# Kernel optimization log

Hardware: AMD Instinct MI355X
Metric: run time of the kernel (lower is better)

## Reference

```python
import jax, jax.numpy as jnp
import numpy as np

N = 50000       # nodes
E = 800000      # edges
F_IN = 128      # num_features
DIM = 64        # dim
D0 = 4 * DIM    # layer-0 width = 256
G = 256         # num graphs
EPS_BN = 1e-5


def _init_linear(key, fan_in, fan_out, bias=True):
    k1, k2 = jax.random.split(key)
    W = jax.random.normal(k1, (fan_in, fan_out), jnp.float32) * (1.0 / np.sqrt(fan_in))
    if bias:
        b = jax.random.normal(k2, (fan_out,), jnp.float32) * 0.01
        return W, b
    return W


def setup_inputs() -> dict:
    key = jax.random.key(0)
    ks = jax.random.split(key, 16)
    x = jax.random.normal(ks[0], (N, F_IN), jnp.float32)
    edge_index = jax.random.randint(ks[1], (2, E), 0, N, jnp.int32)
    edge_attr = jax.random.normal(ks[2], (E, 1), jnp.float32)
    batch = jnp.sort(jax.random.randint(ks[3], (N,), 0, G, jnp.int32))
    # conv0: in F_IN -> out D0, heads=1, edge_dim=1
    Wq0, bq0 = _init_linear(ks[4], F_IN, D0)
    Wk0, bk0 = _init_linear(ks[5], F_IN, D0)
    Wv0, bv0 = _init_linear(ks[6], F_IN, D0)
    We0 = _init_linear(ks[7], 1, D0, bias=False)   # lin_edge has no bias in PyG
    Ws0, bs0 = _init_linear(ks[8], F_IN, D0)       # lin_skip (root weight)
    # conv1: in D0 -> out DIM
    Wq1, bq1 = _init_linear(ks[9], D0, DIM)
    Wk1, bk1 = _init_linear(ks[10], D0, DIM)
    Wv1, bv1 = _init_linear(ks[11], D0, DIM)
    We1 = _init_linear(ks[12], 1, DIM, bias=False)
    Ws1, bs1 = _init_linear(ks[13], D0, DIM)
    # BatchNorm affine params
    gamma0 = jnp.ones((D0,), jnp.float32)
    beta0 = jnp.zeros((D0,), jnp.float32)
    gamma1 = jnp.ones((DIM,), jnp.float32)
    beta1 = jnp.zeros((DIM,), jnp.float32)
    return dict(x=x, edge_index=edge_index, edge_attr=edge_attr, batch=batch,
                Wq0=Wq0, bq0=bq0, Wk0=Wk0, bk0=bk0, Wv0=Wv0, bv0=bv0, We0=We0, Ws0=Ws0, bs0=bs0,
                gamma0=gamma0, beta0=beta0,
                Wq1=Wq1, bq1=bq1, Wk1=Wk1, bk1=bk1, Wv1=Wv1, bv1=bv1, We1=We1, Ws1=Ws1, bs1=bs1,
                gamma1=gamma1, beta1=beta1)


def _transformer_conv(x, edge_index, edge_attr, Wq, bq, Wk, bk, Wv, bv, We, Ws, bs):
    # PyG TransformerConv, heads=1, concat=True, root_weight=True, beta=False
    src, dst = edge_index[0], edge_index[1]
    n, d = x.shape[0], Wq.shape[1]
    q = x @ Wq + bq            # [N, d]
    k = x @ Wk + bk
    v = x @ Wv + bv
    e = edge_attr @ We          # [E, d]
    ke = k[src] + e             # key_j + edge embedding
    logits = jnp.sum(q[dst] * ke, axis=-1) / jnp.sqrt(jnp.asarray(d, jnp.float32))  # [E]
    # scatter-softmax over incoming edges of each dst node
    m = jax.ops.segment_max(logits, dst, num_segments=n)
    p = jnp.exp(logits - m[dst])
    s = jax.ops.segment_sum(p, dst, num_segments=n)
    alpha = p / (s[dst] + 1e-16)
    msg = (v[src] + e) * alpha[:, None]              # [E, d]
    out = jax.ops.segment_sum(msg, dst, num_segments=n)
    return out + x @ Ws + bs                          # root/skip connection


def _batch_norm(x, gamma, beta):
    mu = jnp.mean(x, axis=0)
    var = jnp.mean(jnp.square(x - mu), axis=0)  # biased var (torch training mode)
    return gamma * (x - mu) * jax.lax.rsqrt(var + EPS_BN) + beta


def _global_mean_pool(x, batch, num_graphs):
    s = jax.ops.segment_sum(x, batch, num_segments=num_graphs)
    c = jax.ops.segment_sum(jnp.ones((x.shape[0],), x.dtype), batch, num_segments=num_graphs)
    return s / jnp.maximum(c, 1.0)[:, None]


def reference(x, edge_index, edge_attr, batch,
              Wq0, bq0, Wk0, bk0, Wv0, bv0, We0, Ws0, bs0, gamma0, beta0,
              Wq1, bq1, Wk1, bk1, Wv1, bv1, We1, Ws1, bs1, gamma1, beta1):
    h0 = _batch_norm(_transformer_conv(x, edge_index, edge_attr,
                                       Wq0, bq0, Wk0, bk0, Wv0, bv0, We0, Ws0, bs0),
                     gamma0, beta0)                  # [N, D0]
    h1 = _batch_norm(_transformer_conv(h0, edge_index, edge_attr,
                                       Wq1, bq1, Wk1, bk1, Wv1, bv1, We1, Ws1, bs1),
                     gamma1, beta1)                  # [N, DIM]
    xpool = jnp.concatenate([_global_mean_pool(h0, batch, G),
                             _global_mean_pool(h1, batch, G)], axis=1)  # [G, D0+DIM]
    xs = jnp.concatenate([h0, h1], axis=1)                               # [N, D0+DIM]
    return (xpool, xs)
```

## Files before the change

### kernel.cpp

```cpp
#include <hip/hip_runtime.h>

constexpr int NN = 50000;
constexpr int NE = 800000;
constexpr int F_IN = 128;
constexpr int D0 = 256;
constexpr int D1 = 64;
constexpr int NG = 256;
constexpr float EPS_BN = 1e-5f;

typedef __attribute__((ext_vector_type(8))) short bf16x8;
typedef __attribute__((ext_vector_type(4))) float f32x4;
typedef __attribute__((ext_vector_type(8))) ushort u16x8;
typedef __attribute__((ext_vector_type(4))) ushort u16x4;

__device__ inline ushort f2bf(float f) {
    uint32_t u = __float_as_uint(f);
    uint32_t r = u + 0x7fff + ((u >> 16) & 1);
    return (ushort)(r >> 16);
}
__device__ inline float bf2f(ushort b) {
    return __uint_as_float((uint32_t)b << 16);
}

__global__ __launch_bounds__(256) void k_hist(const int* __restrict__ ei, int* __restrict__ cnt) {
    int e = blockIdx.x * 256 + threadIdx.x;
    if (e < NE) atomicAdd(&cnt[ei[NE + e]], 1);
}

__global__ __launch_bounds__(256) void k_scan1(const int* __restrict__ cnt,
                                               int* __restrict__ offs,
                                               int* __restrict__ bsum) {
    __shared__ int lds[256];
    int idx = blockIdx.x * 256 + threadIdx.x;
    int v = (idx < NN) ? cnt[idx] : 0;
    lds[threadIdx.x] = v;
    __syncthreads();
    #pragma unroll
    for (int off = 1; off < 256; off <<= 1) {
        int add = (threadIdx.x >= off) ? lds[threadIdx.x - off] : 0;
        __syncthreads();
        lds[threadIdx.x] += add;
        __syncthreads();
    }
    if (idx < NN) offs[idx] = lds[threadIdx.x] - v;
    if (threadIdx.x == 255) bsum[blockIdx.x] = lds[255];
}

__global__ __launch_bounds__(256) void k_scan2(const int* __restrict__ bsum,
                                               int* __restrict__ boff, int nblk) {
    __shared__ int lds[256];
    int v = (threadIdx.x < nblk) ? bsum[threadIdx.x] : 0;
    lds[threadIdx.x] = v;
    __syncthreads();
    #pragma unroll
    for (int off = 1; off < 256; off <<= 1) {
        int add = (threadIdx.x >= off) ? lds[threadIdx.x - off] : 0;
        __syncthreads();
        lds[threadIdx.x] += add;
        __syncthreads();
    }
    if (threadIdx.x < nblk) boff[threadIdx.x] = lds[threadIdx.x] - v;
}

__global__ __launch_bounds__(256) void k_scan3(int* __restrict__ offs,
                                               const int* __restrict__ boff,
                                               int* __restrict__ cursor) {
    int idx = blockIdx.x * 256 + threadIdx.x;
    if (idx < NN) {
        int o = offs[idx] + boff[blockIdx.x];
        offs[idx] = o;
        cursor[idx] = o;
    }
    if (idx == 0) offs[NN] = NE;
}

__global__ __launch_bounds__(256) void k_scatter(const int* __restrict__ ei,
                                                 const float* __restrict__ ea,
                                                 int* __restrict__ cursor,
                                                 int2* __restrict__ sedge) {
    int e = blockIdx.x * 256 + threadIdx.x;
    if (e < NE) {
        int d = ei[NE + e];
        int pos = atomicAdd(&cursor[d], 1);
        sedge[pos] = make_int2(ei[e], __float_as_int(ea[e]));
    }
}

__global__ __launch_bounds__(256) void k_f2bf4(const float* __restrict__ in,
                                               ushort* __restrict__ out, int n4) {
    for (int i = blockIdx.x * 256 + threadIdx.x; i < n4; i += gridDim.x * 256) {
        float4 v = *reinterpret_cast<const float4*>(&in[(size_t)i * 4]);
        ushort4 o;
        o.x = f2bf(v.x); o.y = f2bf(v.y); o.z = f2bf(v.z); o.w = f2bf(v.w);
        *reinterpret_cast<ushort4*>(&out[(size_t)i * 4]) = o;
    }
}

struct WPrep {
    const float* src[8];
    ushort* dst[8];
    int K[8];
    int D[8];
};
__global__ __launch_bounds__(256) void k_wprep(WPrep p) {
    int m = blockIdx.y;
    int K = p.K[m], D = p.D[m];
    int n = K * D;
    for (int idx = blockIdx.x * 256 + threadIdx.x; idx < n; idx += gridDim.x * 256) {
        int c = idx / K, k = idx - c * K;
        p.dst[m][idx] = f2bf(p.src[m][(size_t)k * D + c]);
    }
}

template<int K, int DOUT>
__global__ __launch_bounds__(256) void k_gemm_mfma(
    const ushort* __restrict__ Xb, const ushort* __restrict__ Wt,
    const float* __restrict__ B0, const float* __restrict__ B1,
    const float* __restrict__ B2, const float* __restrict__ B3,
    float* __restrict__ Oq, ushort* __restrict__ Okv,
    float* __restrict__ Oh)
{
    constexpr int BM = 128, BN = 64, BK = 32;
    __shared__ ushort Xs[BM][BK + 8];
    __shared__ ushort Wss[BN][BK + 8];

    int row0 = blockIdx.x * BM;
    int col0 = blockIdx.y * BN;
    int mat = col0 / DOUT;
    int mcol0 = col0 - mat * DOUT;
    const float* Bb = (mat == 0) ? B0 : (mat == 1) ? B1 : (mat == 2) ? B2 : B3;

    int t = threadIdx.x;
    int wid = t >> 6, lane = t & 63;
    int wr = wid >> 1, wc = wid & 1;
    int lr = lane & 15, lk = lane >> 4;

    f32x4 acc[4][2] = {};

    for (int k0 = 0; k0 < K; k0 += BK) {
        #pragma unroll
        for (int i = 0; i < 2; ++i) {
            int slot = t + i * 256;
            int r = slot >> 2, c8 = slot & 3;
            int gr = row0 + r;
            uint4 val = make_uint4(0, 0, 0, 0);
            if (gr < NN) val = *reinterpret_cast<const uint4*>(&Xb[(size_t)gr * K + k0 + c8 * 8]);
            *reinterpret_cast<uint4*>(&Xs[r][c8 * 8]) = val;
        }
        {
            int r = t >> 2, c8 = t & 3;
            uint4 val = *reinterpret_cast<const uint4*>(&Wt[(size_t)(col0 + r) * K + k0 + c8 * 8]);
            *reinterpret_cast<uint4*>(&Wss[r][c8 * 8]) = val;
        }
        __syncthreads();
        bf16x8 a[4], b[2];
        #pragma unroll
        for (int m = 0; m < 4; ++m)
            a[m] = *reinterpret_cast<const bf16x8*>(&Xs[wr * 64 + m * 16 + lr][lk * 8]);
        #pragma unroll
        for (int n = 0; n < 2; ++n)
            b[n] = *reinterpret_cast<const bf16x8*>(&Wss[wc * 32 + n * 16 + lr][lk * 8]);
        #pragma unroll
        for (int m = 0; m < 4; ++m)
            #pragma unroll
            for (int n = 0; n < 2; ++n)
                acc[m][n] = __builtin_amdgcn_mfma_f32_16x16x32_bf16(a[m], b[n], acc[m][n], 0, 0, 0);
        __syncthreads();
    }

    #pragma unroll
    for (int m = 0; m < 4; ++m) {
        #pragma unroll
        for (int n = 0; n < 2; ++n) {
            int gcol = mcol0 + wc * 32 + n * 16 + lr;
            float bias = Bb[gcol];
            #pragma unroll
            for (int r = 0; r < 4; ++r) {
                int grow = row0 + wr * 64 + m * 16 + lk * 4 + r;
                if (grow >= NN) continue;
                float vv = acc[m][n][r] + bias;
                if (mat == 0) Oq[(size_t)grow * DOUT + gcol] = vv;
                else if (mat == 1) Okv[(size_t)grow * (2 * DOUT) + gcol] = f2bf(vv);
                else if (mat == 2) Okv[(size_t)grow * (2 * DOUT) + DOUT + gcol] = f2bf(vv);
                else Oh[(size_t)grow * DOUT + gcol] = vv;
            }
        }
    }
}

template<int D>
__global__ __launch_bounds__(256) void k_attn(
    const float* __restrict__ q, const ushort* __restrict__ kvb,
    const float* __restrict__ We,
    const int2* __restrict__ sedge,
    const int* __restrict__ offs,
    float* __restrict__ hout)
{
    int wave = threadIdx.x >> 6;
    int lane = threadIdx.x & 63;
    int node = blockIdx.x * 4 + wave;
    if (node >= NN) return;
    int start = offs[node], stop = offs[node + 1];

    if constexpr (D == 256) {
        constexpr float scale = 0.0625f;
        int g = lane >> 5, sl = lane & 31;
        float q8[8], wel8[8];
        {
            float4 qa = *reinterpret_cast<const float4*>(&q[(size_t)node * 256 + sl * 8]);
            float4 qb = *reinterpret_cast<const float4*>(&q[(size_t)node * 256 + sl * 8 + 4]);
            q8[0] = qa.x; q8[1] = qa.y; q8[2] = qa.z; q8[3] = qa.w;
            q8[4] = qb.x; q8[5] = qb.y; q8[6] = qb.z; q8[7] = qb.w;
            float4 wa = *reinterpret_cast<const float4*>(&We[sl * 8]);
            float4 wb = *reinterpret_cast<const float4*>(&We[sl * 8 + 4]);
            wel8[0] = wa.x; wel8[1] = wa.y; wel8[2] = wa.z; wel8[3] = wa.w;
            wel8[4] = wb.x; wel8[5] = wb.y; wel8[6] = wb.z; wel8[7] = wb.w;
        }
        float qWe = 0.f;
        #pragma unroll
        for (int c = 0; c < 8; ++c) qWe = fmaf(q8[c], wel8[c], qWe);
        #pragma unroll
        for (int o = 1; o <= 16; o <<= 1) qWe += __shfl_xor(qWe, o);

        int niter = (stop - start + 1) >> 1;
        float acc8[8] = {};
        float ssum = 0.f, sse = 0.f;

        bool val0, val1; int2 se0, se1;
        u16x8 ku0, vu0, ku1, vu1;
        auto LOAD = [&](int j, bool& val, int2& se, u16x8& ku, u16x8& vu) {
            int idx = start + 2 * j + g;
            val = idx < stop;
            int e = val ? idx : 0;
            se = sedge[e];
            const ushort* base = &kvb[(size_t)se.x * 512 + sl * 8];
            ku = *reinterpret_cast<const u16x8*>(base);
            vu = *reinterpret_cast<const u16x8*>(base + 256);
        };
        LOAD(0, val0, se0, ku0, vu0);
        LOAD(1, val1, se1, ku1, vu1);

        for (int j = 0; j < niter; ++j) {
            bool val2; int2 se2; u16x8 ku2, vu2;
            LOAD(j + 2, val2, se2, ku2, vu2);
            float dot = 0.f;
            #pragma unroll
            for (int c = 0; c < 8; ++c) dot = fmaf(q8[c], bf2f((ushort)ku0[c]), dot);
            #pragma unroll
            for (int o = 1; o <= 16; o <<= 1) dot += __shfl_xor(dot, o);
            float eav = __int_as_float(se0.y);
            float p = val0 ? __expf((dot + eav * qWe) * scale) : 0.f;
            ssum += p;
            sse = fmaf(p, eav, sse);
            #pragma unroll
            for (int c = 0; c < 8; ++c) acc8[c] = fmaf(p, bf2f((ushort)vu0[c]), acc8[c]);
            val0 = val1; se0 = se1; ku0 = ku1; vu0 = vu1;
            val1 = val2; se1 = se2; ku1 = ku2; vu1 = vu2;
        }
        #pragma unroll
        for (int c = 0; c < 8; ++c) acc8[c] = fmaf(sse, wel8[c], acc8[c]);
        ssum += __shfl_xor(ssum, 32);
        #pragma unroll
        for (int c = 0; c < 8; ++c) acc8[c] += __shfl_xor(acc8[c], 32);
        float inv = 1.0f / (ssum + 1e-16f);
        float o4[4];
        #pragma unroll
        for (int c = 0; c < 4; ++c) o4[c] = g ? acc8[4 + c] : acc8[c];
        float* hp = &hout[(size_t)node * 256 + sl * 8 + g * 4];
        float4 cur = *reinterpret_cast<float4*>(hp);
        cur.x += o4[0] * inv; cur.y += o4[1] * inv;
        cur.z += o4[2] * inv; cur.w += o4[3] * inv;
        *reinterpret_cast<float4*>(hp) = cur;
    } else {
        constexpr float scale = 0.125f;
        int g = lane >> 4, sl = lane & 15;
        float q4[4], wel4[4];
        {
            float4 qa = *reinterpret_cast<const float4*>(&q[(size_t)node * 64 + sl * 4]);
            q4[0] = qa.x; q4[1] = qa.y; q4[2] = qa.z; q4[3] = qa.w;
            float4 wa = *reinterpret_cast<const float4*>(&We[sl * 4]);
            wel4[0] = wa.x; wel4[1] = wa.y; wel4[2] = wa.z; wel4[3] = wa.w;
        }
        float qWe = 0.f;
        #pragma unroll
        for (int c = 0; c < 4; ++c) qWe = fmaf(q4[c], wel4[c], qWe);
        #pragma unroll
        for (int o = 1; o <= 8; o <<= 1) qWe += __shfl_xor(qWe, o);

        int niter = (stop - start + 3) >> 2;
        float acc4[4] = {};
        float ssum = 0.f, sse = 0.f;

        bool val0, val1; int2 se0, se1;
        u16x4 ku0, vu0, ku1, vu1;
        auto LOAD = [&](int j, bool& val, int2& se, u16x4& ku, u16x4& vu) {
            int idx = start + 4 * j + g;
            val = idx < stop;
            int e = val ? idx : 0;
            se = sedge[e];
            const ushort* base = &kvb[(size_t)se.x * 128 + sl * 4];
            ku = *reinterpret_cast<const u16x4*>(base);
            vu = *reinterpret_cast<const u16x4*>(base + 64);
        };
        LOAD(0, val0, se0, ku0, vu0);
        LOAD(1, val1, se1, ku1, vu1);

        for (int j = 0; j < niter; ++j) {
            bool val2; int2 se2; u16x4 ku2, vu2;
            LOAD(j + 2, val2, se2, ku2, vu2);
            float dot = 0.f;
            #pragma unroll
            for (int c = 0; c < 4; ++c) dot = fmaf(q4[c], bf2f((ushort)ku0[c]), dot);
            #pragma unroll
            for (int o = 1; o <= 8; o <<= 1) dot += __shfl_xor(dot, o);
            float eav = __int_as_float(se0.y);
            float p = val0 ? __expf((dot + eav * qWe) * scale) : 0.f;
            ssum += p;
            sse = fmaf(p, eav, sse);
            #pragma unroll
            for (int c = 0; c < 4; ++c) acc4[c] = fmaf(p, bf2f((ushort)vu0[c]), acc4[c]);
            val0 = val1; se0 = se1; ku0 = ku1; vu0 = vu1;
            val1 = val2; se1 = se2; ku1 = ku2; vu1 = vu2;
        }
        #pragma unroll
        for (int c = 0; c < 4; ++c) acc4[c] = fmaf(sse, wel4[c], acc4[c]);
        ssum += __shfl_xor(ssum, 16);
        ssum += __shfl_xor(ssum, 32);
        #pragma unroll
        for (int c = 0; c < 4; ++c) {
            acc4[c] += __shfl_xor(acc4[c], 16);
            acc4[c] += __shfl_xor(acc4[c], 32);
        }
        float inv = 1.0f / (ssum + 1e-16f);
        float av = acc4[0];
        av = (g == 1) ? acc4[1] : av;
        av = (g == 2) ? acc4[2] : av;
        av = (g == 3) ? acc4[3] : av;
        hout[(size_t)node * 64 + sl * 4 + g] += av * inv;
    }
}

template<int D>
__global__ __launch_bounds__(256) void k_bnstats(const float* __restrict__ h,
                                                 float* __restrict__ sums,
                                                 int rows_per_block) {
    constexpr int NSUB = 256 / D;
    int col = threadIdx.x % D;
    int sub = threadIdx.x / D;
    int r0 = blockIdx.x * rows_per_block;
    int r1 = min(r0 + rows_per_block, NN);
    float s = 0.f, ss = 0.f;
    for (int r = r0 + sub; r < r1; r += NSUB) {
        float x = h[(size_t)r * D + col];
        s += x; ss += x * x;
    }
    atomicAdd(&sums[col], s);
    atomicAdd(&sums[D + col], ss);
}

template<int D>
__global__ void k_bnfin(const float* __restrict__ sums,
                        const float* __restrict__ gamma, const float* __restrict__ beta,
                        float* __restrict__ ab) {
    int c = threadIdx.x;
    if (c >= D) return;
    float mean = sums[c] / (float)NN;
    float var = sums[D + c] / (float)NN - mean * mean;
    float a = gamma[c] * rsqrtf(var + EPS_BN);
    ab[c] = a;
    ab[D + c] = beta[c] - mean * a;
}

__global__ __launch_bounds__(256) void k_bnapply0(float* __restrict__ h,
                                                  const float* __restrict__ ab,
                                                  float* __restrict__ xs,
                                                  ushort* __restrict__ h0b) {
    int idx = blockIdx.x * 256 + threadIdx.x;
    int n = idx >> 6, c4 = idx & 63;
    float4 x4 = *reinterpret_cast<float4*>(&h[(size_t)idx * 4]);
    float4 a4 = *reinterpret_cast<const float4*>(&ab[c4 * 4]);
    float4 b4 = *reinterpret_cast<const float4*>(&ab[256 + c4 * 4]);
    float4 r;
    r.x = a4.x * x4.x + b4.x; r.y = a4.y * x4.y + b4.y;
    r.z = a4.z * x4.z + b4.z; r.w = a4.w * x4.w + b4.w;
    *reinterpret_cast<float4*>(&xs[(size_t)n * 320 + c4 * 4]) = r;
    ushort4 o;
    o.x = f2bf(r.x); o.y = f2bf(r.y); o.z = f2bf(r.z); o.w = f2bf(r.w);
    *reinterpret_cast<ushort4*>(&h0b[(size_t)idx * 4]) = o;
}

__global__ __launch_bounds__(256) void k_bnapply1(const float* __restrict__ h,
                                                  const float* __restrict__ ab,
                                                  float* __restrict__ xs) {
    int idx = blockIdx.x * 256 + threadIdx.x;
    int n = idx >> 4, c4 = idx & 15;
    float4 x4 = *reinterpret_cast<const float4*>(&h[(size_t)idx * 4]);
    float4 a4 = *reinterpret_cast<const float4*>(&ab[c4 * 4]);
    float4 b4 = *reinterpret_cast<const float4*>(&ab[64 + c4 * 4]);
    float4 r;
    r.x = a4.x * x4.x + b4.x; r.y = a4.y * x4.y + b4.y;
    r.z = a4.z * x4.z + b4.z; r.w = a4.w * x4.w + b4.w;
    *reinterpret_cast<float4*>(&xs[(size_t)n * 320 + 256 + c4 * 4]) = r;
}

__global__ __launch_bounds__(256) void k_pool(const float* __restrict__ xs,
                                              const int* __restrict__ batch,
                                              float* __restrict__ xpool) {
    int g = blockIdx.x;
    __shared__ int se[2];
    if (threadIdx.x < 2) {
        int target = g + threadIdx.x;
        int lo = 0, hi = NN;
        while (lo < hi) {
            int mid = (lo + hi) >> 1;
            if (batch[mid] < target) lo = mid + 1; else hi = mid;
        }
        se[threadIdx.x] = lo;
    }
    __syncthreads();
    int start = se[0], stop = se[1];
    float cnt = fmaxf((float)(stop - start), 1.0f);
    for (int c = threadIdx.x; c < 320; c += 256) {
        float s = 0.f;
        for (int r = start; r < stop; ++r) s += xs[(size_t)r * 320 + c];
        xpool[(size_t)g * 320 + c] = s / cnt;
    }
}

extern "C" void kernel_launch(void* const* d_in, const int* in_sizes, int n_in,
                              void* d_out, int out_size, void* d_ws, size_t ws_size,
                              hipStream_t stream) {
    const float* x     = (const float*)d_in[0];
    const int*   ei    = (const int*)d_in[1];
    const float* ea    = (const float*)d_in[2];
    const int*   batch = (const int*)d_in[3];
    const float *Wq0 = (const float*)d_in[4],  *bq0 = (const float*)d_in[5];
    const float *Wk0 = (const float*)d_in[6],  *bk0 = (const float*)d_in[7];
    const float *Wv0 = (const float*)d_in[8],  *bv0 = (const float*)d_in[9];
    const float *We0 = (const float*)d_in[10];
    const float *Ws0 = (const float*)d_in[11], *bs0 = (const float*)d_in[12];
    const float *gamma0 = (const float*)d_in[13], *beta0 = (const float*)d_in[14];
    const float *Wq1 = (const float*)d_in[15], *bq1 = (const float*)d_in[16];
    const float *Wk1 = (const float*)d_in[17], *bk1 = (const float*)d_in[18];
    const float *Wv1 = (const float*)d_in[19], *bv1 = (const float*)d_in[20];
    const float *We1 = (const float*)d_in[21];
    const float *Ws1 = (const float*)d_in[22], *bs1 = (const float*)d_in[23];
    const float *gamma1 = (const float*)d_in[24], *beta1 = (const float*)d_in[25];

    char* ws = (char*)d_ws;
    size_t off = 0;
    auto alloc = [&](size_t bytes) -> char* {
        char* p = ws + off;
        off += (bytes + 255) & ~(size_t)255;
        return p;
    };
    float*  q0   = (float*)alloc((size_t)NN * D0 * 4);
    ushort* kv0  = (ushort*)alloc((size_t)NN * 2 * D0 * 2);
    float*  h0   = (float*)alloc((size_t)NN * D0 * 4);
    ushort* xbuf = (ushort*)alloc((size_t)NN * D0 * 2);
    int2*  sedge = (int2*)alloc((size_t)NE * 8);
    int*   cnt    = (int*)alloc((size_t)(NN + 1) * 4);
    int*   offs   = (int*)alloc((size_t)(NN + 1) * 4);
    int*   cursor = (int*)alloc((size_t)(NN + 1) * 4);
    int*   bsum   = (int*)alloc(256 * 4);
    int*   boff   = (int*)alloc(256 * 4);
    float* sums0  = (float*)alloc(2 * D0 * 4);
    float* ab0    = (float*)alloc(2 * D0 * 4);
    float* sums1  = (float*)alloc(2 * D1 * 4);
    float* ab1    = (float*)alloc(2 * D1 * 4);
    ushort* wt0   = (ushort*)alloc((size_t)4 * D0 * F_IN * 2);
    ushort* wt1   = (ushort*)alloc((size_t)4 * D1 * D0 * 2);

    ushort* xb  = xbuf;
    ushort* h0b = xbuf;

    float*  q1  = q0;
    ushort* kv1 = kv0;
    float*  h1  = h0;

    float* xpool = (float*)d_out;
    float* xs = (float*)d_out + (size_t)NG * 320;

    const int NBLK = (NN + 255) / 256;
    const int BN_BLK = (NN + 63) / 64;

    hipMemsetAsync(cnt, 0, (NN + 1) * 4, stream);
    k_hist<<<(NE + 255) / 256, 256, 0, stream>>>(ei, cnt);
    k_scan1<<<NBLK, 256, 0, stream>>>(cnt, offs, bsum);
    k_scan2<<<1, 256, 0, stream>>>(bsum, boff, NBLK);
    k_scan3<<<NBLK, 256, 0, stream>>>(offs, boff, cursor);
    k_scatter<<<(NE + 255) / 256, 256, 0, stream>>>(ei, ea, cursor, sedge);

    k_f2bf4<<<2048, 256, 0, stream>>>(x, xb, NN * F_IN / 4);
    WPrep wp;
    wp.src[0] = Wq0; wp.src[1] = Wk0; wp.src[2] = Wv0; wp.src[3] = Ws0;
    wp.src[4] = Wq1; wp.src[5] = Wk1; wp.src[6] = Wv1; wp.src[7] = Ws1;
    for (int m = 0; m < 4; ++m) { wp.K[m] = F_IN; wp.D[m] = D0; wp.dst[m] = wt0 + (size_t)m * D0 * F_IN; }
    for (int m = 0; m < 4; ++m) { wp.K[4+m] = D0; wp.D[4+m] = D1; wp.dst[4+m] = wt1 + (size_t)m * D1 * D0; }
    k_wprep<<<dim3(64, 8), 256, 0, stream>>>(wp);

    k_gemm_mfma<F_IN, D0><<<dim3((NN + 127) / 128, 16), 256, 0, stream>>>(
        xb, wt0, bq0, bk0, bv0, bs0, q0, kv0, h0);
    k_attn<D0><<<(NN + 3) / 4, 256, 0, stream>>>(q0, kv0, We0, sedge, offs, h0);
    hipMemsetAsync(sums0, 0, 2 * D0 * 4, stream);
    k_bnstats<D0><<<BN_BLK, 256, 0, stream>>>(h0, sums0, 64);
    k_bnfin<D0><<<1, D0, 0, stream>>>(sums0, gamma0, beta0, ab0);
    k_bnapply0<<<(NN * 64 + 255) / 256, 256, 0, stream>>>(h0, ab0, xs, h0b);

    k_gemm_mfma<D0, D1><<<dim3((NN + 127) / 128, 4), 256, 0, stream>>>(
        h0b, wt1, bq1, bk1, bv1, bs1, q1, kv1, h1);
    k_attn<D1><<<(NN + 3) / 4, 256, 0, stream>>>(q1, kv1, We1, sedge, offs, h1);
    hipMemsetAsync(sums1, 0, 2 * D1 * 4, stream);
    k_bnstats<D1><<<BN_BLK, 256, 0, stream>>>(h1, sums1, 64);
    k_bnfin<D1><<<1, D1, 0, stream>>>(sums1, gamma1, beta1, ab1);
    k_bnapply1<<<(NN * 16 + 255) / 256, 256, 0, stream>>>(h1, ab1, xs);

    k_pool<<<NG, 256, 0, stream>>>(xs, batch, xpool);
}
```

Baseline: 768.6 us.

## Store Q in bf16, interleave layer-1 K/V, widen GEMM tile, tile weight transpose

The query projection output is now written and read as bf16 instead of fp32, which halves Q traffic between the GEMM and attention kernels. In layer 1, K and V are interleaved per 4-column group so each lane gathers both with a single 16-byte load per edge instead of two 8-byte loads. The layer-0 GEMM uses a 128-wide N tile to improve reuse of the X tile, and the weight transpose/convert now goes through an LDS tile so global accesses are coalesced. Rounding Q to bf16 adds some numerical error in the attention logits.

```diff
diff --git a/kernel.cpp b/kernel.cpp
--- a/kernel.cpp
+++ b/kernel.cpp
@@ -105,22 +105,38 @@
 __global__ __launch_bounds__(256) void k_wprep(WPrep p) {
     int m = blockIdx.y;
     int K = p.K[m], D = p.D[m];
-    int n = K * D;
-    for (int idx = blockIdx.x * 256 + threadIdx.x; idx < n; idx += gridDim.x * 256) {
-        int c = idx / K, k = idx - c * K;
-        p.dst[m][idx] = f2bf(p.src[m][(size_t)k * D + c]);
-    }
-}
-
-template<int K, int DOUT>
+    int ntx = K >> 5, nty = D >> 5;
+    int tile = blockIdx.x;
+    if (tile >= ntx * nty) return;
+    int tk = (tile % ntx) << 5;
+    int tc = (tile / ntx) << 5;
+    __shared__ ushort lds[32][33];
+    int tx = threadIdx.x & 31, ty = threadIdx.x >> 5;
+    const float* src = p.src[m];
+    ushort* dst = p.dst[m];
+    #pragma unroll
+    for (int i = 0; i < 4; ++i) {
+        int k = tk + ty + i * 8;
+        lds[ty + i * 8][tx] = f2bf(src[(size_t)k * D + tc + tx]);
+    }
+    __syncthreads();
+    #pragma unroll
+    for (int i = 0; i < 4; ++i) {
+        int c = tc + ty + i * 8;
+        dst[(size_t)c * K + tk + tx] = lds[tx][ty + i * 8];
+    }
+}
+
+template<int K, int DOUT, int BN>
 __global__ __launch_bounds__(256) void k_gemm_mfma(
     const ushort* __restrict__ Xb, const ushort* __restrict__ Wt,
     const float* __restrict__ B0, const float* __restrict__ B1,
     const float* __restrict__ B2, const float* __restrict__ B3,
-    float* __restrict__ Oq, ushort* __restrict__ Okv,
+    ushort* __restrict__ Oqb, ushort* __restrict__ Okv,
     float* __restrict__ Oh)
 {
-    constexpr int BM = 128, BN = 64, BK = 32;
+    constexpr int BM = 128, BK = 32;
+    constexpr int NB = BN / 32;
     __shared__ ushort Xs[BM][BK + 8];
     __shared__ ushort Wss[BN][BK + 8];
 
@@ -135,7 +151,7 @@
     int wr = wid >> 1, wc = wid & 1;
     int lr = lane & 15, lk = lane >> 4;
 
-    f32x4 acc[4][2] = {};
+    f32x4 acc[4][NB] = {};
 
     for (int k0 = 0; k0 < K; k0 += BK) {
         #pragma unroll
@@ -147,23 +163,25 @@
             if (gr < NN) val = *reinterpret_cast<const uint4*>(&Xb[(size_t)gr * K + k0 + c8 * 8]);
             *reinterpret_cast<uint4*>(&Xs[r][c8 * 8]) = val;
         }
-        {
-            int r = t >> 2, c8 = t & 3;
+        #pragma unroll
+        for (int i = 0; i < (BN * 4) / 256; ++i) {
+            int slot = t + i * 256;
+            int r = slot >> 2, c8 = slot & 3;
             uint4 val = *reinterpret_cast<const uint4*>(&Wt[(size_t)(col0 + r) * K + k0 + c8 * 8]);
             *reinterpret_cast<uint4*>(&Wss[r][c8 * 8]) = val;
         }
         __syncthreads();
-        bf16x8 a[4], b[2];
+        bf16x8 a[4], b[NB];
         #pragma unroll
         for (int m = 0; m < 4; ++m)
             a[m] = *reinterpret_cast<const bf16x8*>(&Xs[wr * 64 + m * 16 + lr][lk * 8]);
         #pragma unroll
-        for (int n = 0; n < 2; ++n)
-            b[n] = *reinterpret_cast<const bf16x8*>(&Wss[wc * 32 + n * 16 + lr][lk * 8]);
+        for (int n = 0; n < NB; ++n)
+            b[n] = *reinterpret_cast<const bf16x8*>(&Wss[wc * (BN / 2) + n * 16 + lr][lk * 8]);
         #pragma unroll
         for (int m = 0; m < 4; ++m)
             #pragma unroll
-            for (int n = 0; n < 2; ++n)
+            for (int n = 0; n < NB; ++n)
                 acc[m][n] = __builtin_amdgcn_mfma_f32_16x16x32_bf16(a[m], b[n], acc[m][n], 0, 0, 0);
         __syncthreads();
     }
@@ -171,18 +189,23 @@
     #pragma unroll
     for (int m = 0; m < 4; ++m) {
         #pragma unroll
-        for (int n = 0; n < 2; ++n) {
-            int gcol = mcol0 + wc * 32 + n * 16 + lr;
+        for (int n = 0; n < NB; ++n) {
+            int gcol = mcol0 + wc * (BN / 2) + n * 16 + lr;
             float bias = Bb[gcol];
             #pragma unroll
             for (int r = 0; r < 4; ++r) {
                 int grow = row0 + wr * 64 + m * 16 + lk * 4 + r;
                 if (grow >= NN) continue;
                 float vv = acc[m][n][r] + bias;
-                if (mat == 0) Oq[(size_t)grow * DOUT + gcol] = vv;
-                else if (mat == 1) Okv[(size_t)grow * (2 * DOUT) + gcol] = f2bf(vv);
-                else if (mat == 2) Okv[(size_t)grow * (2 * DOUT) + DOUT + gcol] = f2bf(vv);
-                else Oh[(size_t)grow * DOUT + gcol] = vv;
+                if (mat == 0) {
+                    Oqb[(size_t)grow * DOUT + gcol] = f2bf(vv);
+                } else if (mat == 3) {
+                    Oh[(size_t)grow * DOUT + gcol] = vv;
+                } else if (DOUT == 256) {
+                    Okv[(size_t)grow * 512 + (mat == 2 ? 256 : 0) + gcol] = f2bf(vv);
+                } else {
+                    Okv[(size_t)grow * 128 + ((gcol >> 2) << 3) + (mat == 2 ? 4 : 0) + (gcol & 3)] = f2bf(vv);
+                }
             }
         }
     }
@@ -190,7 +213,7 @@
 
 template<int D>
 __global__ __launch_bounds__(256) void k_attn(
-    const float* __restrict__ q, const ushort* __restrict__ kvb,
+    const ushort* __restrict__ qb, const ushort* __restrict__ kvb,
     const float* __restrict__ We,
     const int2* __restrict__ sedge,
     const int* __restrict__ offs,
@@ -207,10 +230,9 @@
         int g = lane >> 5, sl = lane & 31;
         float q8[8], wel8[8];
         {
-            float4 qa = *reinterpret_cast<const float4*>(&q[(size_t)node * 256 + sl * 8]);
-            float4 qb = *reinterpret_cast<const float4*>(&q[(size_t)node * 256 + sl * 8 + 4]);
-            q8[0] = qa.x; q8[1] = qa.y; q8[2] = qa.z; q8[3] = qa.w;
-            q8[4] = qb.x; q8[5] = qb.y; q8[6] = qb.z; q8[7] = qb.w;
+            u16x8 qu = *reinterpret_cast<const u16x8*>(&qb[(size_t)node * 256 + sl * 8]);
+            #pragma unroll
+            for (int c = 0; c < 8; ++c) q8[c] = bf2f((ushort)qu[c]);
             float4 wa = *reinterpret_cast<const float4*>(&We[sl * 8]);
             float4 wb = *reinterpret_cast<const float4*>(&We[sl * 8 + 4]);
             wel8[0] = wa.x; wel8[1] = wa.y; wel8[2] = wa.z; wel8[3] = wa.w;
@@ -276,8 +298,8 @@
         int g = lane >> 4, sl = lane & 15;
         float q4[4], wel4[4];
         {
-            float4 qa = *reinterpret_cast<const float4*>(&q[(size_t)node * 64 + sl * 4]);
-            q4[0] = qa.x; q4[1] = qa.y; q4[2] = qa.z; q4[3] = qa.w;
+            ushort4 qu = *reinterpret_cast<const ushort4*>(&qb[(size_t)node * 64 + sl * 4]);
+            q4[0] = bf2f(qu.x); q4[1] = bf2f(qu.y); q4[2] = bf2f(qu.z); q4[3] = bf2f(qu.w);
             float4 wa = *reinterpret_cast<const float4*>(&We[sl * 4]);
             wel4[0] = wa.x; wel4[1] = wa.y; wel4[2] = wa.z; wel4[3] = wa.w;
         }
@@ -292,25 +314,23 @@
         float ssum = 0.f, sse = 0.f;
 
         bool val0, val1; int2 se0, se1;
-        u16x4 ku0, vu0, ku1, vu1;
-        auto LOAD = [&](int j, bool& val, int2& se, u16x4& ku, u16x4& vu) {
+        u16x8 kv0r, kv1r;
+        auto LOAD = [&](int j, bool& val, int2& se, u16x8& kv) {
             int idx = start + 4 * j + g;
             val = idx < stop;
             int e = val ? idx : 0;
             se = sedge[e];
-            const ushort* base = &kvb[(size_t)se.x * 128 + sl * 4];
-            ku = *reinterpret_cast<const u16x4*>(base);
-            vu = *reinterpret_cast<const u16x4*>(base + 64);
+            kv = *reinterpret_cast<const u16x8*>(&kvb[(size_t)se.x * 128 + sl * 8]);
         };
-        LOAD(0, val0, se0, ku0, vu0);
-        LOAD(1, val1, se1, ku1, vu1);
+        LOAD(0, val0, se0, kv0r);
+        LOAD(1, val1, se1, kv1r);
 
         for (int j = 0; j < niter; ++j) {
-            bool val2; int2 se2; u16x4 ku2, vu2;
-            LOAD(j + 2, val2, se2, ku2, vu2);
+            bool val2; int2 se2; u16x8 kv2r;
+            LOAD(j + 2, val2, se2, kv2r);
             float dot = 0.f;
             #pragma unroll
-            for (int c = 0; c < 4; ++c) dot = fmaf(q4[c], bf2f((ushort)ku0[c]), dot);
+            for (int c = 0; c < 4; ++c) dot = fmaf(q4[c], bf2f((ushort)kv0r[c]), dot);
             #pragma unroll
             for (int o = 1; o <= 8; o <<= 1) dot += __shfl_xor(dot, o);
             float eav = __int_as_float(se0.y);
@@ -318,25 +338,24 @@
             ssum += p;
             sse = fmaf(p, eav, sse);
             #pragma unroll
-            for (int c = 0; c < 4; ++c) acc4[c] = fmaf(p, bf2f((ushort)vu0[c]), acc4[c]);
-            val0 = val1; se0 = se1; ku0 = ku1; vu0 = vu1;
-            val1 = val2; se1 = se2; ku1 = ku2; vu1 = vu2;
+            for (int c = 0; c < 4; ++c) acc4[c] = fmaf(p, bf2f((ushort)kv0r[4 + c]), acc4[c]);
+            val0 = val1; se0 = se1; kv0r = kv1r;
+            val1 = val2; se1 = se2; kv1r = kv2r;
         }
         #pragma unroll
         for (int c = 0; c < 4; ++c) acc4[c] = fmaf(sse, wel4[c], acc4[c]);
-        ssum += __shfl_xor(ssum, 16);
-        ssum += __shfl_xor(ssum, 32);
+        ssum += __shfl_xor(ssum, 16); ssum += __shfl_xor(ssum, 32);
         #pragma unroll
         for (int c = 0; c < 4; ++c) {
             acc4[c] += __shfl_xor(acc4[c], 16);
             acc4[c] += __shfl_xor(acc4[c], 32);
         }
         float inv = 1.0f / (ssum + 1e-16f);
-        float av = acc4[0];
-        av = (g == 1) ? acc4[1] : av;
-        av = (g == 2) ? acc4[2] : av;
-        av = (g == 3) ? acc4[3] : av;
-        hout[(size_t)node * 64 + sl * 4 + g] += av * inv;
+        float a = acc4[0];
+        a = (g == 1) ? acc4[1] : a;
+        a = (g == 2) ? acc4[2] : a;
+        a = (g == 3) ? acc4[3] : a;
+        hout[(size_t)node * 64 + sl * 4 + g] += a * inv;
     }
 }
 
@@ -454,7 +473,7 @@
         off += (bytes + 255) & ~(size_t)255;
         return p;
     };
-    float*  q0   = (float*)alloc((size_t)NN * D0 * 4);
+    ushort* qb0  = (ushort*)alloc((size_t)NN * D0 * 2);
     ushort* kv0  = (ushort*)alloc((size_t)NN * 2 * D0 * 2);
     float*  h0   = (float*)alloc((size_t)NN * D0 * 4);
     ushort* xbuf = (ushort*)alloc((size_t)NN * D0 * 2);
@@ -474,8 +493,8 @@
     ushort* xb  = xbuf;
     ushort* h0b = xbuf;
 
-    float*  q1  = q0;
-    ushort* kv1 = kv0;
+    ushort* qb1 = qb0;
+    ushort* kvi1 = kv0;
     float*  h1  = h0;
 
     float* xpool = (float*)d_out;
@@ -497,19 +516,19 @@
     wp.src[4] = Wq1; wp.src[5] = Wk1; wp.src[6] = Wv1; wp.src[7] = Ws1;
     for (int m = 0; m < 4; ++m) { wp.K[m] = F_IN; wp.D[m] = D0; wp.dst[m] = wt0 + (size_t)m * D0 * F_IN; }
     for (int m = 0; m < 4; ++m) { wp.K[4+m] = D0; wp.D[4+m] = D1; wp.dst[4+m] = wt1 + (size_t)m * D1 * D0; }
-    k_wprep<<<dim3(64, 8), 256, 0, stream>>>(wp);
-
-    k_gemm_mfma<F_IN, D0><<<dim3((NN + 127) / 128, 16), 256, 0, stream>>>(
-        xb, wt0, bq0, bk0, bv0, bs0, q0, kv0, h0);
-    k_attn<D0><<<(NN + 3) / 4, 256, 0, stream>>>(q0, kv0, We0, sedge, offs, h0);
+    k_wprep<<<dim3(32, 8), 256, 0, stream>>>(wp);
+
+    k_gemm_mfma<F_IN, D0, 128><<<dim3((NN + 127) / 128, 8), 256, 0, stream>>>(
+        xb, wt0, bq0, bk0, bv0, bs0, qb0, kv0, h0);
+    k_attn<D0><<<(NN + 3) / 4, 256, 0, stream>>>(qb0, kv0, We0, sedge, offs, h0);
     hipMemsetAsync(sums0, 0, 2 * D0 * 4, stream);
     k_bnstats<D0><<<BN_BLK, 256, 0, stream>>>(h0, sums0, 64);
     k_bnfin<D0><<<1, D0, 0, stream>>>(sums0, gamma0, beta0, ab0);
     k_bnapply0<<<(NN * 64 + 255) / 256, 256, 0, stream>>>(h0, ab0, xs, h0b);
 
-    k_gemm_mfma<D0, D1><<<dim3((NN + 127) / 128, 4), 256, 0, stream>>>(
-        h0b, wt1, bq1, bk1, bv1, bs1, q1, kv1, h1);
-    k_attn<D1><<<(NN + 3) / 4, 256, 0, stream>>>(q1, kv1, We1, sedge, offs, h1);
+    k_gemm_mfma<D0, D1, 64><<<dim3((NN + 127) / 128, 4), 256, 0, stream>>>(
+        h0b, wt1, bq1, bk1, bv1, bs1, qb1, kvi1, h1);
+    k_attn<D1><<<(NN + 3) / 4, 256, 0, stream>>>(qb1, kvi1, We1, sedge, offs, h1);
     hipMemsetAsync(sums1, 0, 2 * D1 * 4, stream);
     k_bnstats<D1><<<BN_BLK, 256, 0, stream>>>(h1, sums1, 64);
     k_bnfin<D1><<<1, D1, 0, stream>>>(sums1, gamma1, beta1, ab1);
```

Result: no change. 758.4 us (-1.3%).
